# Kernel optimization log

Hardware: AMD Instinct MI355X
Metric: run time of the kernel (lower is better)

## Reference

```python
import jax, jax.numpy as jnp
import numpy as np

D_MODEL, D_INNER, D_STATE, DT_RANK, D_CONV = 1024, 2048, 16, 64, 4
B, L = 2, 2048


def setup_inputs() -> dict:
    key = jax.random.key(0)
    ks = jax.random.split(key, 14)
    s = lambda k, shp, fan: jax.random.normal(k, shp, jnp.float32) / np.sqrt(fan)
    return {
        "resid": jax.random.normal(ks[0], (B, L, D_MODEL), jnp.float32),
        "norm_w": jnp.ones((D_MODEL,), jnp.float32),
        "skip_w": s(ks[1], (D_INNER, D_MODEL), D_MODEL),
        "in_w": s(ks[2], (D_INNER, D_MODEL), D_MODEL),
        "conv_w": s(ks[3], (D_INNER, D_CONV), D_CONV),
        "conv_b": jnp.zeros((D_INNER,), jnp.float32),
        "wd1": s(ks[4], (DT_RANK, D_INNER), D_INNER),
        "wd2": s(ks[5], (D_INNER, DT_RANK), DT_RANK),
        "wd2_b": jnp.zeros((D_INNER,), jnp.float32),
        "wb": s(ks[6], (D_STATE, D_INNER), D_INNER),
        "wc": s(ks[7], (D_STATE, D_INNER), D_INNER),
        "A_log": jax.random.normal(ks[8], (D_INNER, D_STATE), jnp.float32),
        "W_D": jnp.ones((D_INNER,), jnp.float32),
        "out_w": s(ks[9], (D_MODEL, D_INNER), D_INNER),
    }


def _rmsnorm(x, w, eps=1e-5):
    return x * jax.lax.rsqrt(jnp.mean(x * x, axis=-1, keepdims=True) + eps) * w


def _causal_depthwise_conv(x, conv_w, conv_b):
    # x: (B, L, E); conv_w: (E, K). Torch Conv1d padding=K-1 then slice [:L] == causal left pad.
    K = conv_w.shape[1]
    xp = jnp.pad(x, ((0, 0), (K - 1, 0), (0, 0)))
    Lx = x.shape[1]
    out = conv_b
    for k in range(K):
        out = out + xp[:, k:k + Lx, :] * conv_w[:, k]
    return out


def _selective_scan(x, delta, Bm, Cm, A):
    # x, delta: (B, L, E); Bm, Cm: (B, L, N); A: (E, N)
    h0 = jnp.zeros((x.shape[0], A.shape[0], A.shape[1]), x.dtype)

    def step(h, inp):
        xt, dt, bt, ct = inp  # (B,E), (B,E), (B,N), (B,N)
        A_bar = jnp.exp(dt[..., None] * A)                      # (B,E,N)
        h = A_bar * h + (dt * xt)[..., None] * bt[:, None, :]   # (B,E,N)
        y = jnp.einsum('ben,bn->be', h, ct)
        return h, y

    xs = tuple(jnp.swapaxes(a, 0, 1) for a in (x, delta, Bm, Cm))
    _, ys = jax.lax.scan(step, h0, xs)
    return jnp.swapaxes(ys, 0, 1)  # (B, L, E)


def reference(resid, norm_w, skip_w, in_w, conv_w, conv_b, wd1, wd2, wd2_b, wb, wc, A_log, W_D, out_w):
    x = _rmsnorm(resid, norm_w)
    skip = x @ skip_w.T                       # (B,L,E)
    x = x @ in_w.T                            # (B,L,E)
    x = _causal_depthwise_conv(x, conv_w, conv_b)
    x = jax.nn.silu(x)
    A = -jnp.exp(A_log)                       # (E,N)
    delta = jax.nn.softplus((x @ wd1.T) @ wd2.T + wd2_b)  # (B,L,E)
    Bm = x @ wb.T                             # (B,L,N)
    Cm = x @ wc.T                             # (B,L,N)
    y = _selective_scan(x, delta, Bm, Cm, A)
    y = y + x * W_D
    y = y * jax.nn.silu(skip)
    y = y @ out_w.T                           # (B,L,D)
    return resid + y
```

## Files before the change

### kernel.cpp

```cpp
#include <hip/hip_runtime.h>
#include <stdint.h>

typedef unsigned short u16;
typedef unsigned int u32;
typedef __bf16 bf16x8 __attribute__((ext_vector_type(8)));
typedef u16 u16x8 __attribute__((ext_vector_type(8)));
typedef float f32x4 __attribute__((ext_vector_type(4)));

#define LOG2E 1.44269504088896340736f

__device__ __forceinline__ u16 f2bf(float f) {
  u32 u = __float_as_uint(f);
  u += 0x7fffu + ((u >> 16) & 1u);
  return (u16)(u >> 16);
}
__device__ __forceinline__ float bf2f(u16 s) { return __uint_as_float(((u32)s) << 16); }
__device__ __forceinline__ float fexp2(float x) { return __builtin_amdgcn_exp2f(x); }

struct alignas(8) U16x4 { u16 x, y, z, w; };

__device__ __forceinline__ void load_lds16(const u16* g, u16* l) {
  __builtin_amdgcn_global_load_lds((const __attribute__((address_space(1))) void*)g,
                                   (__attribute__((address_space(3))) void*)l, 16, 0, 0);
}

struct CvtArgs {
  const float* src[8];
  u16* dst[8];
  int cnt4[8];
  int total4;
};

__global__ __launch_bounds__(256) void cvt8_kernel(CvtArgs a) {
  for (int g = blockIdx.x * 256 + threadIdx.x; g < a.total4; g += gridDim.x * 256) {
    int i = 0, off = g;
    while (off >= a.cnt4[i]) { off -= a.cnt4[i]; ++i; }
    float4 v = make_float4(0.f, 0.f, 0.f, 0.f);
    if (a.src[i]) v = ((const float4*)a.src[i])[off];
    U16x4 o;
    o.x = f2bf(v.x); o.y = f2bf(v.y); o.z = f2bf(v.z); o.w = f2bf(v.w);
    ((U16x4*)a.dst[i])[off] = o;
  }
}

__global__ __launch_bounds__(256) void cvt_t96_kernel(const float* __restrict__ src,
                                                      u16* __restrict__ dst) {
  const int g = blockIdx.x * 256 + threadIdx.x;
  const float4 v = ((const float4*)src)[g];
  U16x4 o;
  o.x = f2bf(v.x); o.y = f2bf(v.y); o.z = f2bf(v.z); o.w = f2bf(v.w);
  ((U16x4*)dst)[g] = o;
}

__global__ __launch_bounds__(256) void rmsnorm_kernel(const float* __restrict__ resid,
                                                      const float* __restrict__ w,
                                                      u16* __restrict__ xn) {
  const int row = blockIdx.x;
  const int tid = threadIdx.x;
  const float4 v = ((const float4*)(resid + (size_t)row * 1024))[tid];
  float ss = v.x * v.x + v.y * v.y + v.z * v.z + v.w * v.w;
#pragma unroll
  for (int off = 32; off > 0; off >>= 1) ss += __shfl_down(ss, off, 64);
  __shared__ float red[4];
  const int lane = tid & 63, wid = tid >> 6;
  if (lane == 0) red[wid] = ss;
  __syncthreads();
  const float tot = red[0] + red[1] + red[2] + red[3];
  const float sc = rsqrtf(tot * (1.0f / 1024.0f) + 1e-5f);
  const float4 wv = ((const float4*)w)[tid];
  U16x4 o;
  o.x = f2bf(v.x * sc * wv.x); o.y = f2bf(v.y * sc * wv.y);
  o.z = f2bf(v.z * sc * wv.z); o.w = f2bf(v.w * sc * wv.w);
  ((U16x4*)(xn + (size_t)row * 1024))[tid] = o;
}

template <int EPI>
__global__ __launch_bounds__(256) void gemm_bt(
    const u16* __restrict__ A, const u16* __restrict__ Bw,
    void* __restrict__ C1, void* __restrict__ C2,
    const float* __restrict__ bias,
    int Kslice, int lda, int ldb, int ldc, int split, int nstore) {
  __shared__ alignas(16) u16 As[128 * 32];
  __shared__ alignas(16) u16 Bs[128 * 32];
  const int tid = threadIdx.x;
  const int lane = tid & 63, wid = tid >> 6;
  const int wr = wid >> 1, wcid = wid & 1;

  int bx, by;
  {
    const int gy = gridDim.y;
    const int flat = blockIdx.y * 32 + blockIdx.x;
    if ((gy & 3) == 0) {
      const int xcd = flat & 7, idx = flat >> 3;
      const int sy = gy >> 2;
      bx = (xcd & 1) * 16 + (idx & 15);
      by = (xcd >> 1) * sy + (idx >> 4);
    } else { bx = blockIdx.x; by = blockIdx.y; }
  }

  const long brow = (long)bx * 128, bcol = (long)by * 128;
  const int kt0 = blockIdx.z * Kslice;

  f32x4 acc[4][4] = {};

  const int srow = tid >> 2;
  const int scol = ((tid & 3) ^ ((srow >> 1) & 3)) * 8;
  const u16* Ag = A + (brow + srow) * (long)lda + scol;
  const u16* Bg = Bw + (bcol + srow) * (long)ldb + scol;
  u16* Asp = As + tid * 8;
  u16* Bsp = Bs + tid * 8;
  const int fr = lane & 15;
  const int kk2 = (((lane >> 4) ^ ((lane >> 1) & 3))) * 8;

  for (int kt = kt0; kt < kt0 + Kslice; kt += 32) {
    __syncthreads();
    load_lds16(Ag + kt, Asp);
    load_lds16(Ag + kt + 64L * lda, Asp + 64 * 32);
    load_lds16(Bg + kt, Bsp);
    load_lds16(Bg + kt + 64L * ldb, Bsp + 64 * 32);
    __syncthreads();
    bf16x8 af[4], bfr[4];
#pragma unroll
    for (int i = 0; i < 4; ++i) {
      af[i]  = *(const bf16x8*)(As + (wr * 64 + i * 16 + fr) * 32 + kk2);
      bfr[i] = *(const bf16x8*)(Bs + (wcid * 64 + i * 16 + fr) * 32 + kk2);
    }
#pragma unroll
    for (int i = 0; i < 4; ++i)
#pragma unroll
      for (int j = 0; j < 4; ++j)
        acc[i][j] = __builtin_amdgcn_mfma_f32_16x16x32_bf16(af[i], bfr[j], acc[i][j], 0, 0, 0);
  }

  const int fq = lane >> 4;
#pragma unroll
  for (int i = 0; i < 4; ++i) {
#pragma unroll
    for (int j = 0; j < 4; ++j) {
      const long col = bcol + wcid * 64 + j * 16 + fr;
      if ((int)col < nstore) {
#pragma unroll
        for (int r = 0; r < 4; ++r) {
          const long row = brow + wr * 64 + i * 16 + fq * 4 + r;
          float v = acc[i][j][r];
          if (EPI == 1) {
            v += bias[col];
            v = fmaxf(v, 0.f) + log1pf(__expf(-fabsf(v)));
          }
          if (EPI == 4) {
            atomicAdd((float*)C1 + row * ldc + col, v);
          } else if ((int)col < split) {
            ((u16*)C1)[row * ldc + col] = f2bf(v);
          } else {
            ((u16*)C2)[row * ldc + (col - split)] = f2bf(v);
          }
        }
      }
    }
  }
}

__global__ __launch_bounds__(256) void conv_silu_kernel(
    const u16* __restrict__ u, const float* __restrict__ cw, const float* __restrict__ cb,
    u16* __restrict__ xc) {
  const int row = blockIdx.x;
  const int l = row & 2047;
  const int t = threadIdx.x;
  const int e0 = t * 8;
  const size_t base = (size_t)row * 2048 + e0;
  bf16x8 xv[4];
#pragma unroll
  for (int k = 0; k < 4; ++k) {
    const int ls = l - 3 + k;
    if (ls >= 0) xv[k] = *(const bf16x8*)(u + base + (long)(k - 3) * 2048);
    else { bf16x8 z = {}; xv[k] = z; }
  }
  u16x8 o;
#pragma unroll
  for (int j = 0; j < 8; ++j) {
    const int e = e0 + j;
    const float4 w = ((const float4*)cw)[e];
    float acc = cb[e];
    acc = fmaf(w.x, (float)xv[0][j], acc);
    acc = fmaf(w.y, (float)xv[1][j], acc);
    acc = fmaf(w.z, (float)xv[2][j], acc);
    acc = fmaf(w.w, (float)xv[3][j], acc);
    const float s = acc / (1.f + __expf(-acc));
    o[j] = f2bf(s);
  }
  *(u16x8*)(xc + base) = o;
}

__global__ __launch_bounds__(256) void scan_p1(
    const u16* __restrict__ delta, const u16* __restrict__ xc, const u16* __restrict__ t96,
    const float* __restrict__ A_log, float* __restrict__ P, float* __restrict__ H) {
  const int tid = threadIdx.x;
  const int e = blockIdx.x * 256 + tid;
  const int c = blockIdx.y, b = blockIdx.z;
  __shared__ alignas(16) u16 Dsh[32 * 256];
  __shared__ alignas(16) u16 Xsh[32 * 256];
  __shared__ float Bsh[32][16];
  const size_t rowbase = ((size_t)(b * 2048 + c * 32)) * 2048 + blockIdx.x * 256;
#pragma unroll
  for (int k = 0; k < 4; ++k) {
    const int i = tid + k * 256;
    const size_t go = rowbase + (size_t)(i >> 5) * 2048 + (i & 31) * 8;
    load_lds16(delta + go, Dsh + i * 8);
    load_lds16(xc + go, Xsh + i * 8);
  }
  for (int i = tid; i < 512; i += 256) {
    const int l0 = i >> 4, n = i & 15;
    Bsh[l0][n] = bf2f(t96[(size_t)(b * 2048 + c * 32 + l0) * 96 + 64 + n]);
  }
  float kv[16], h[16];
#pragma unroll
  for (int n = 0; n < 16; ++n) {
    kv[n] = -__expf(A_log[(size_t)e * 16 + n]) * LOG2E;
    h[n] = 0.f;
  }
  __syncthreads();
  float sdt = 0.f;
  for (int l0 = 0; l0 < 32; ++l0) {
    const float dt = bf2f(Dsh[l0 * 256 + tid]);
    const float x  = bf2f(Xsh[l0 * 256 + tid]);
    const float dtx = dt * x;
    sdt += dt;
#pragma unroll
    for (int n = 0; n < 16; ++n) {
      const float ab = fexp2(kv[n] * dt);
      h[n] = fmaf(ab, h[n], dtx * Bsh[l0][n]);
    }
  }
  const size_t o0 = (((size_t)(b * 64 + c)) * 16) * 2048 + e;
#pragma unroll
  for (int n = 0; n < 16; ++n) {
    P[o0 + (size_t)n * 2048] = fexp2(kv[n] * sdt);
    H[o0 + (size_t)n * 2048] = h[n];
  }
}

__global__ __launch_bounds__(256) void scan_p2(float* __restrict__ P, float* __restrict__ H) {
  const int g = blockIdx.x * 256 + threadIdx.x;
  const int e = g & 2047;
  const int n = (g >> 11) & 15;
  const int b = g >> 15;
  const size_t base = (((size_t)(b * 64)) * 16 + n) * 2048 + e;
  float h = 0.f;
  for (int c = 0; c < 64; ++c) {
    const size_t a = base + (size_t)c * (16 * 2048);
    const float Pc = P[a], hl = H[a];
    H[a] = h;
    h = fmaf(Pc, h, hl);
  }
}

__global__ __launch_bounds__(256) void scan_p3(
    const u16* __restrict__ delta, const u16* __restrict__ xc, const u16* __restrict__ t96,
    const float* __restrict__ A_log, const float* __restrict__ Hin,
    const u16* __restrict__ skip, const float* __restrict__ W_D, u16* __restrict__ ybar) {
  const int tid = threadIdx.x;
  const int e = blockIdx.x * 256 + tid;
  const int c = blockIdx.y, b = blockIdx.z;
  __shared__ alignas(16) u16 Dsh[32 * 256];
  __shared__ alignas(16) u16 Xsh[32 * 256];
  __shared__ float Bsh[32][16], Csh[32][16];
  const size_t rowbase = ((size_t)(b * 2048 + c * 32)) * 2048 + blockIdx.x * 256;
#pragma unroll
  for (int k = 0; k < 4; ++k) {
    const int i = tid + k * 256;
    const size_t go = rowbase + (size_t)(i >> 5) * 2048 + (i & 31) * 8;
    load_lds16(delta + go, Dsh + i * 8);
    load_lds16(xc + go, Xsh + i * 8);
  }
  for (int i = tid; i < 512; i += 256) {
    const int l0 = i >> 4, n = i & 15;
    const size_t rowo = (size_t)(b * 2048 + c * 32 + l0) * 96;
    Bsh[l0][n] = bf2f(t96[rowo + 64 + n]);
    Csh[l0][n] = bf2f(t96[rowo + 80 + n]);
  }
  float kv[16], h[16];
  const size_t o0 = (((size_t)(b * 64 + c)) * 16) * 2048 + e;
#pragma unroll
  for (int n = 0; n < 16; ++n) {
    kv[n] = -__expf(A_log[(size_t)e * 16 + n]) * LOG2E;
    h[n] = Hin[o0 + (size_t)n * 2048];
  }
  const float wd = W_D[e];
  __syncthreads();
  const size_t base = ((size_t)(b * 2048 + c * 32)) * 2048 + e;
  for (int l0 = 0; l0 < 32; ++l0) {
    const float dt = bf2f(Dsh[l0 * 256 + tid]);
    const float x  = bf2f(Xsh[l0 * 256 + tid]);
    const float dtx = dt * x;
    float y = 0.f;
#pragma unroll
    for (int n = 0; n < 16; ++n) {
      const float ab = fexp2(kv[n] * dt);
      h[n] = fmaf(ab, h[n], dtx * Bsh[l0][n]);
      y = fmaf(h[n], Csh[l0][n], y);
    }
    y = fmaf(x, wd, y);
    const float s = bf2f(skip[base + (size_t)l0 * 2048]);
    y *= s / (1.f + __expf(-s));
    ybar[base + (size_t)l0 * 2048] = f2bf(y);
  }
}

extern "C" void kernel_launch(void* const* d_in, const int* in_sizes, int n_in,
                              void* d_out, int out_size, void* d_ws, size_t ws_size,
                              hipStream_t stream) {
  const float* resid  = (const float*)d_in[0];
  const float* norm_w = (const float*)d_in[1];
  const float* skip_w = (const float*)d_in[2];
  const float* in_w   = (const float*)d_in[3];
  const float* conv_w = (const float*)d_in[4];
  const float* conv_b = (const float*)d_in[5];
  const float* wd1    = (const float*)d_in[6];
  const float* wd2    = (const float*)d_in[7];
  const float* wd2_b  = (const float*)d_in[8];
  const float* wb     = (const float*)d_in[9];
  const float* wc     = (const float*)d_in[10];
  const float* A_log  = (const float*)d_in[11];
  const float* W_D    = (const float*)d_in[12];
  const float* out_w  = (const float*)d_in[13];
  float* out = (float*)d_out;

  char* ws = (char*)d_ws;
  u16* w_in   = (u16*)(ws + 0);
  u16* w_skip = (u16*)(ws + 4194304);
  u16* w_out  = (u16*)(ws + 8388608);
  u16* w_wd2  = (u16*)(ws + 12582912);
  u16* w2cat  = (u16*)(ws + 12845056);
  u16* xn     = (u16*)(ws + 13369344);
  u16* u      = (u16*)(ws + 21757952);
  u16* delta  = u;
  u16* skip   = (u16*)(ws + 38535168);
  u16* xc     = (u16*)(ws + 55312384);
  u16* t96    = (u16*)(ws + 72089600);
  float* P    = (float*)(ws + 72876032);
  float* t96f = (float*)(ws + 72876032);
  u16* ybar   = (u16*)(ws + 72876032);
  float* H    = (float*)(ws + 89653248);

  CvtArgs ca{};
  ca.src[0] = in_w;   ca.dst[0] = w_in;              ca.cnt4[0] = 2097152 / 4;
  ca.src[1] = skip_w; ca.dst[1] = w_skip;            ca.cnt4[1] = 2097152 / 4;
  ca.src[2] = out_w;  ca.dst[2] = w_out;             ca.cnt4[2] = 2097152 / 4;
  ca.src[3] = wd2;    ca.dst[3] = w_wd2;             ca.cnt4[3] = 131072 / 4;
  ca.src[4] = wd1;    ca.dst[4] = w2cat;             ca.cnt4[4] = 131072 / 4;
  ca.src[5] = wb;     ca.dst[5] = w2cat + 64 * 2048; ca.cnt4[5] = 32768 / 4;
  ca.src[6] = wc;     ca.dst[6] = w2cat + 80 * 2048; ca.cnt4[6] = 32768 / 4;
  ca.src[7] = nullptr;ca.dst[7] = w2cat + 96 * 2048; ca.cnt4[7] = 65536 / 4;
  ca.total4 = (2097152 * 3 + 131072 * 2 + 32768 * 2 + 65536) / 4;
  cvt8_kernel<<<2048, 256, 0, stream>>>(ca);

  rmsnorm_kernel<<<4096, 256, 0, stream>>>(resid, norm_w, xn);

  gemm_bt<0><<<dim3(32, 32), 256, 0, stream>>>(xn, w_in, u, skip, nullptr,
                                               1024, 1024, 1024, 2048, 2048, 4096);

  conv_silu_kernel<<<4096, 256, 0, stream>>>(u, conv_w, conv_b, xc);

  hipMemsetAsync(t96f, 0, 4096 * 96 * 4, stream);
  gemm_bt<4><<<dim3(32, 1, 4), 256, 0, stream>>>(xc, w2cat, t96f, nullptr, nullptr,
                                                 512, 2048, 2048, 96, 1 << 30, 96);
  cvt_t96_kernel<<<384, 256, 0, stream>>>(t96f, t96);

  gemm_bt<1><<<dim3(32, 16), 256, 0, stream>>>(t96, w_wd2, delta, nullptr, wd2_b,
                                               64, 96, 64, 2048, 1 << 30, 2048);

  scan_p1<<<dim3(8, 64, 2), 256, 0, stream>>>(delta, xc, t96, A_log, P, H);
  scan_p2<<<256, 256, 0, stream>>>(P, H);
  scan_p3<<<dim3(8, 64, 2), 256, 0, stream>>>(delta, xc, t96, A_log, H, skip, W_D, ybar);

  hipMemcpyAsync(out, resid, 4096 * 1024 * 4, hipMemcpyDeviceToDevice, stream);
  gemm_bt<4><<<dim3(32, 8, 2), 256, 0, stream>>>(ybar, w_out, out, nullptr, nullptr,
                                                 1024, 2048, 2048, 1024, 1 << 30, 1024);
}
```

Measured before the change: 374.2 us.

## Double-buffer GEMM LDS tiles and fuse residual add into output GEMM

Changes the shared GEMM to use two LDS buffers, so global-to-LDS loads for the next K tile are issued while MFMAs run on the current one, which also removes one barrier per iteration. The final out-projection no longer copies resid into out and split-K accumulates with atomics. It now runs without a K split and writes acc plus resid directly in a new epilogue. This halves that GEMM's grid, from 512 to 256 blocks, and doubles LDS per block, which may lower occupancy.

```diff
diff --git a/kernel.cpp b/kernel.cpp
--- a/kernel.cpp
+++ b/kernel.cpp
@@ -78,10 +78,10 @@
 __global__ __launch_bounds__(256) void gemm_bt(
     const u16* __restrict__ A, const u16* __restrict__ Bw,
     void* __restrict__ C1, void* __restrict__ C2,
-    const float* __restrict__ bias,
+    const float* __restrict__ bias, const float* __restrict__ resid,
     int Kslice, int lda, int ldb, int ldc, int split, int nstore) {
-  __shared__ alignas(16) u16 As[128 * 32];
-  __shared__ alignas(16) u16 Bs[128 * 32];
+  __shared__ alignas(16) u16 As[2][128 * 32];
+  __shared__ alignas(16) u16 Bs[2][128 * 32];
   const int tid = threadIdx.x;
   const int lane = tid & 63, wid = tid >> 6;
   const int wr = wid >> 1, wcid = wid & 1;
@@ -100,6 +100,7 @@
 
   const long brow = (long)bx * 128, bcol = (long)by * 128;
   const int kt0 = blockIdx.z * Kslice;
+  const int nt = Kslice >> 5;
 
   f32x4 acc[4][4] = {};
 
@@ -107,29 +108,43 @@
   const int scol = ((tid & 3) ^ ((srow >> 1) & 3)) * 8;
   const u16* Ag = A + (brow + srow) * (long)lda + scol;
   const u16* Bg = Bw + (bcol + srow) * (long)ldb + scol;
-  u16* Asp = As + tid * 8;
-  u16* Bsp = Bs + tid * 8;
   const int fr = lane & 15;
-  const int kk2 = (((lane >> 4) ^ ((lane >> 1) & 3))) * 8;
-
-  for (int kt = kt0; kt < kt0 + Kslice; kt += 32) {
-    __syncthreads();
-    load_lds16(Ag + kt, Asp);
-    load_lds16(Ag + kt + 64L * lda, Asp + 64 * 32);
-    load_lds16(Bg + kt, Bsp);
-    load_lds16(Bg + kt + 64L * ldb, Bsp + 64 * 32);
-    __syncthreads();
+  const int kk2 = ((lane >> 4) ^ ((lane >> 1) & 3)) * 8;
+
+  {
+    u16* Asp = As[0] + tid * 8;
+    u16* Bsp = Bs[0] + tid * 8;
+    load_lds16(Ag + kt0, Asp);
+    load_lds16(Ag + kt0 + 64L * lda, Asp + 64 * 32);
+    load_lds16(Bg + kt0, Bsp);
+    load_lds16(Bg + kt0 + 64L * ldb, Bsp + 64 * 32);
+  }
+  __syncthreads();
+
+  int cur = 0;
+  for (int t = 0; t < nt; ++t) {
+    if (t + 1 < nt) {
+      const int kt = kt0 + (t + 1) * 32;
+      u16* Asp = As[cur ^ 1] + tid * 8;
+      u16* Bsp = Bs[cur ^ 1] + tid * 8;
+      load_lds16(Ag + kt, Asp);
+      load_lds16(Ag + kt + 64L * lda, Asp + 64 * 32);
+      load_lds16(Bg + kt, Bsp);
+      load_lds16(Bg + kt + 64L * ldb, Bsp + 64 * 32);
+    }
     bf16x8 af[4], bfr[4];
 #pragma unroll
     for (int i = 0; i < 4; ++i) {
-      af[i]  = *(const bf16x8*)(As + (wr * 64 + i * 16 + fr) * 32 + kk2);
-      bfr[i] = *(const bf16x8*)(Bs + (wcid * 64 + i * 16 + fr) * 32 + kk2);
+      af[i]  = *(const bf16x8*)(As[cur] + (wr * 64 + i * 16 + fr) * 32 + kk2);
+      bfr[i] = *(const bf16x8*)(Bs[cur] + (wcid * 64 + i * 16 + fr) * 32 + kk2);
     }
 #pragma unroll
     for (int i = 0; i < 4; ++i)
 #pragma unroll
       for (int j = 0; j < 4; ++j)
         acc[i][j] = __builtin_amdgcn_mfma_f32_16x16x32_bf16(af[i], bfr[j], acc[i][j], 0, 0, 0);
+    if (t + 1 < nt) __syncthreads();
+    cur ^= 1;
   }
 
   const int fq = lane >> 4;
@@ -149,6 +164,8 @@
           }
           if (EPI == 4) {
             atomicAdd((float*)C1 + row * ldc + col, v);
+          } else if (EPI == 2) {
+            ((float*)C1)[row * ldc + col] = v + resid[row * ldc + col];
           } else if ((int)col < split) {
             ((u16*)C1)[row * ldc + col] = f2bf(v);
           } else {
@@ -356,24 +373,23 @@
 
   rmsnorm_kernel<<<4096, 256, 0, stream>>>(resid, norm_w, xn);
 
-  gemm_bt<0><<<dim3(32, 32), 256, 0, stream>>>(xn, w_in, u, skip, nullptr,
+  gemm_bt<0><<<dim3(32, 32), 256, 0, stream>>>(xn, w_in, u, skip, nullptr, nullptr,
                                                1024, 1024, 1024, 2048, 2048, 4096);
 
   conv_silu_kernel<<<4096, 256, 0, stream>>>(u, conv_w, conv_b, xc);
 
   hipMemsetAsync(t96f, 0, 4096 * 96 * 4, stream);
-  gemm_bt<4><<<dim3(32, 1, 4), 256, 0, stream>>>(xc, w2cat, t96f, nullptr, nullptr,
+  gemm_bt<4><<<dim3(32, 1, 4), 256, 0, stream>>>(xc, w2cat, t96f, nullptr, nullptr, nullptr,
                                                  512, 2048, 2048, 96, 1 << 30, 96);
   cvt_t96_kernel<<<384, 256, 0, stream>>>(t96f, t96);
 
-  gemm_bt<1><<<dim3(32, 16), 256, 0, stream>>>(t96, w_wd2, delta, nullptr, wd2_b,
+  gemm_bt<1><<<dim3(32, 16), 256, 0, stream>>>(t96, w_wd2, delta, nullptr, wd2_b, nullptr,
                                                64, 96, 64, 2048, 1 << 30, 2048);
 
   scan_p1<<<dim3(8, 64, 2), 256, 0, stream>>>(delta, xc, t96, A_log, P, H);
   scan_p2<<<256, 256, 0, stream>>>(P, H);
   scan_p3<<<dim3(8, 64, 2), 256, 0, stream>>>(delta, xc, t96, A_log, H, skip, W_D, ybar);
 
-  hipMemcpyAsync(out, resid, 4096 * 1024 * 4, hipMemcpyDeviceToDevice, stream);
-  gemm_bt<4><<<dim3(32, 8, 2), 256, 0, stream>>>(ybar, w_out, out, nullptr, nullptr,
-                                                 1024, 2048, 2048, 1024, 1 << 30, 1024);
-}
+  gemm_bt<2><<<dim3(32, 8), 256, 0, stream>>>(ybar, w_out, out, nullptr, nullptr, resid,
+                                              2048, 2048, 2048, 1024, 1 << 30, 1024);
+}
```

After: 345.0 us. -7.8%, faster.
